# Performance work log

Hardware: AMD Instinct MI355X
Metric: run time of the kernel (lower is better)

## Reference

```python
import jax, jax.numpy as jnp
import numpy as np

BATCH, SEQ, DIN, FILTERS, KSIZE = 64, 512, 256, 256, 3

def setup_inputs() -> dict:
    key = jax.random.key(0)
    ks = jax.random.split(key, 5)
    s_u = 1.0 / np.sqrt(DIN)
    return {
        "x": jax.random.normal(ks[0], (BATCH, SEQ, DIN), dtype=jnp.float32),
        "z": jax.random.normal(ks[1], (BATCH, DIN), dtype=jnp.float32),
        "U": jax.random.normal(ks[2], (DIN, DIN), dtype=jnp.float32) * s_u,
        "V": jax.random.normal(ks[3], (DIN, KSIZE * FILTERS), dtype=jnp.float32) * s_u,
        "B_w": jax.random.normal(ks[4], (DIN, KSIZE * FILTERS), dtype=jnp.float32) * s_u,
        "b": jnp.zeros((FILTERS,), dtype=jnp.float32),
        "kernel_size": KSIZE,
    }

def reference(x, z, U, V, B_w, b, kernel_size):
    Bn, L, din = x.shape
    K = int(kernel_size)
    F = V.shape[1] // K
    # per-sample dynamic kernel: (U * sigmoid(z)) @ V + B
    zf = jax.nn.sigmoid(z)                                  # (B, din)
    f = jnp.einsum('de,be,ef->bdf', U, zf, V) + B_w[None]    # (B, din, K*F)
    f = f.reshape(Bn, din, K, F).transpose(0, 2, 1, 3)       # (B, K, din, F)
    # 'same' padding, stride 1
    pad_l, pad_r = (K - 1) // 2, K // 2
    xp = jnp.pad(x, ((0, 0), (pad_l, pad_r), (0, 0)))        # (B, L+K-1, din)
    patches = jnp.stack([xp[:, i:i + L] for i in range(K)], axis=2)  # (B, L, K, din)
    out = jnp.einsum('blkd,bkdf->blf', patches, f) + b       # (B, L, F)
    return jax.nn.relu(out)
```

## Files before the change

kernel.cpp:

```cpp
#include <hip/hip_runtime.h>
#include <math.h>

#define BATCH 64
#define SEQL  512
#define DIN   256
#define NF    256
#define KS    3
#define KF    (KS * NF)

#define XCH 512
#define XL  (SEQL + 2)
#define KC  (KS * XCH)
#define LDR 128
#define AROWS 136

typedef __attribute__((ext_vector_type(8))) short short8;
typedef __attribute__((ext_vector_type(4))) float floatx4;
typedef __attribute__((ext_vector_type(8))) unsigned short ushort8v;

static __device__ __forceinline__ unsigned short f2bf(float f) {
    unsigned int u = __float_as_uint(f);
    return (unsigned short)((u + 0x7FFF + ((u >> 16) & 1)) >> 16);
}

static __device__ __forceinline__ void gl_lds16(const void* g, void* l) {
    __builtin_amdgcn_global_load_lds(
        (const __attribute__((address_space(1))) unsigned int*)g,
        (__attribute__((address_space(3))) unsigned int*)l, 16, 0, 0);
}

template <int NROWS>
static __device__ __forceinline__ void stage_tile(
    const unsigned short* __restrict__ gbase, size_t rs,
    unsigned short* lds, int wave, int lane)
{
    constexpr int WROWS = NROWS / 4;
    const int rsub = lane >> 4;
    const int ud   = lane & 15;
    unsigned short* ldsw = lds + (size_t)(wave * WROWS) * LDR;
    const unsigned short* g = gbase + (size_t)(wave * WROWS) * rs;
    #pragma unroll
    for (int c = 0; c < WROWS / 4; ++c) {
        const int r  = c * 4 + rsub;
        const int ug = ud ^ (r & 15);
        gl_lds16(g + (size_t)r * rs + ug * 8, ldsw + (size_t)(c * 4) * LDR);
    }
}

__global__ __launch_bounds__(256) void pack_kernel(
    const float* __restrict__ U, const float* __restrict__ V,
    const float* __restrict__ Bw,
    unsigned short* __restrict__ WcT, unsigned short* __restrict__ UT,
    unsigned short* __restrict__ Xc)
{
    const int blk = blockIdx.x;
    const int t   = threadIdx.x;
    __shared__ unsigned short tile[64][64 + 2];

    if (blk < 96) {
        const int f0 = (blk & 3) * 64, c0 = (blk >> 2) * 64;
        const int fl = t & 63, cb = t >> 6;
        #pragma unroll
        for (int it = 0; it < 16; ++it) {
            const int cl = cb + it * 4;
            const int c  = c0 + cl;
            const int k  = c >> 9, ch = c & (XCH - 1);
            const float v = (ch < DIN) ? Bw[(size_t)ch * KF + k * NF + f0 + fl]
                                       : V[(size_t)(ch - DIN) * KF + k * NF + f0 + fl];
            tile[cl][fl] = f2bf(v);
        }
        __syncthreads();
        const int cl2 = t & 63, fb = t >> 6;
        #pragma unroll
        for (int it = 0; it < 16; ++it) {
            const int fl2 = fb + it * 4;
            WcT[(size_t)(f0 + fl2) * KC + c0 + cl2] = tile[cl2][fl2];
        }
    } else if (blk < 112) {
        const int bb = blk - 96;
        const int e0 = (bb & 3) * 64, d0 = (bb >> 2) * 64;
        const int el = t & 63, db = t >> 6;
        #pragma unroll
        for (int it = 0; it < 16; ++it) {
            const int dl = db + it * 4;
            tile[dl][el] = f2bf(U[(size_t)(d0 + dl) * DIN + e0 + el]);
        }
        __syncthreads();
        const int dl2 = t & 63, eb = t >> 6;
        #pragma unroll
        for (int it = 0; it < 16; ++it) {
            const int el2 = eb + it * 4;
            UT[(size_t)(e0 + el2) * DIN + d0 + dl2] = tile[dl2][el2];
        }
    } else {
        const int b = blk - 112;
        unsigned int* r0 = (unsigned int*)(Xc + (size_t)b * XL * XCH);
        unsigned int* r1 = (unsigned int*)(Xc + ((size_t)b * XL + XL - 1) * XCH);
        r0[t] = 0u;
        r1[t] = 0u;
    }
}

__global__ __launch_bounds__(256, 4) void stage1_kernel(
    const float* __restrict__ x, const unsigned short* __restrict__ UT,
    const float* __restrict__ z, unsigned short* __restrict__ Xc)
{
    __shared__ unsigned short sh[16384];
    unsigned short* As = sh;
    unsigned short* Bs = sh + 4096;

    const int tid  = threadIdx.x;
    const int lane = tid & 63;
    const int wave = tid >> 6;
    const int quad = lane >> 4, l16 = lane & 15;

    const int bid   = blockIdx.x;
    const int ft    = (bid >> 3) & 1;
    const int mt    = ((bid >> 4) << 3) | (bid & 7);
    const int b     = mt >> 3;
    const int lbase = (mt & 7) * 64;
    const int e0    = ft * 128;
    const bool writeX = (ft == 0);

    const int r8  = lane >> 3;
    const int ud8 = lane & 7;

    floatx4 acc[4][2] = {};

    for (int k0 = 0; k0 < DIN; k0 += 64) {
        #pragma unroll
        for (int c = 0; c < 4; ++c) {
            const int r  = wave * 32 + c * 8 + r8;
            const int ug = ud8 ^ (r & 7);
            gl_lds16(UT + (size_t)(e0 + r) * DIN + k0 + ug * 8,
                     Bs + (size_t)(wave * 32 + c * 8) * 64);
        }
        #pragma unroll
        for (int it = 0; it < 2; ++it) {
            const int idx = tid + it * 256;
            const int row = idx >> 3;
            const int u   = idx & 7;
            const int ug  = u ^ (row & 7);
            const float* xp =
                x + ((size_t)b * SEQL + lbase + row) * DIN + k0 + ug * 8;
            const float4 v0 = *(const float4*)xp;
            const float4 v1 = *(const float4*)(xp + 4);
            ushort8v h;
            h[0] = f2bf(v0.x); h[1] = f2bf(v0.y); h[2] = f2bf(v0.z); h[3] = f2bf(v0.w);
            h[4] = f2bf(v1.x); h[5] = f2bf(v1.y); h[6] = f2bf(v1.z); h[7] = f2bf(v1.w);
            *(ushort8v*)&As[row * 64 + u * 8] = h;
            if (writeX)
                *(ushort8v*)&Xc[((size_t)b * XL + lbase + 1 + row) * XCH + k0 + ug * 8] = h;
        }
        __syncthreads();

        #pragma unroll
        for (int ks = 0; ks < 2; ++ks) {
            short8 af[4], bfr[2];
            #pragma unroll
            for (int i = 0; i < 4; ++i) {
                const int m = i * 16 + l16;
                af[i] = *(const short8*)&As[m * 64 + (((ks * 4 + quad) ^ (l16 & 7)) * 8)];
            }
            #pragma unroll
            for (int j = 0; j < 2; ++j) {
                const int n = wave * 32 + j * 16 + l16;
                bfr[j] = *(const short8*)&Bs[n * 64 + (((ks * 4 + quad) ^ (l16 & 7)) * 8)];
            }
            #pragma unroll
            for (int i = 0; i < 4; ++i)
                #pragma unroll
                for (int j = 0; j < 2; ++j)
                    acc[i][j] = __builtin_amdgcn_mfma_f32_16x16x32_bf16(
                        af[i], bfr[j], acc[i][j], 0, 0, 0);
        }
        __syncthreads();
    }

    #pragma unroll
    for (int j = 0; j < 2; ++j) {
        const int el = wave * 32 + j * 16 + l16;
        const float zf = 1.0f / (1.0f + expf(-z[(size_t)b * DIN + e0 + el]));
        #pragma unroll
        for (int i = 0; i < 4; ++i) {
            const int m = i * 16 + quad * 4;
            #pragma unroll
            for (int r = 0; r < 4; ++r)
                sh[(m + r) * 128 + el] = f2bf(acc[i][j][r] * zf);
        }
    }
    __syncthreads();
    #pragma unroll
    for (int it = 0; it < 4; ++it) {
        const int idx = tid + it * 256;
        const int row = idx >> 4;
        const int u   = idx & 15;
        *(ushort8v*)&Xc[((size_t)b * XL + lbase + 1 + row) * XCH + DIN + e0 + u * 8] =
            *(const ushort8v*)&sh[row * 128 + u * 8];
    }
}

__global__ __launch_bounds__(256, 3) void stage2_kernel(
    const unsigned short* __restrict__ Xc,
    const unsigned short* __restrict__ WcT,
    const float* __restrict__ bias, float* __restrict__ out)
{
    __shared__ unsigned short As[AROWS * LDR];
    __shared__ unsigned short Bs[64 * LDR];

    const int tid  = threadIdx.x;
    const int lane = tid & 63;
    const int wave = tid >> 6;
    const int quad = lane >> 4, l16 = lane & 15;

    const int bid   = blockIdx.x;
    const int ft    = (bid >> 3) & 3;
    const int mt    = ((bid >> 5) << 3) | (bid & 7);
    const int b     = mt >> 2;
    const int lbase = (mt & 3) * 128;
    const int f0    = ft * 64;

    const unsigned short* gA = Xc + ((size_t)b * XL + lbase) * XCH;
    const unsigned short* gB = WcT + (size_t)f0 * KC;

    const int rsub = lane >> 4;
    const int ud   = lane & 15;
    const int wr0   = (wave < 2) ? wave * 36 : 72 + (wave - 2) * 32;
    const int ncall = (wave < 2) ? 9 : 8;

    floatx4 acc[2][4] = {};

    #pragma unroll 1
    for (int g = 0; g < 4; ++g) {
        #pragma unroll
        for (int c = 0; c < 9; ++c) {
            if (c < ncall) {
                const int r  = wr0 + c * 4 + rsub;
                const int ug = ud ^ (r & 15);
                gl_lds16(gA + (size_t)r * XCH + g * 128 + ug * 8,
                         As + (size_t)(wr0 + c * 4) * LDR);
            }
        }
        #pragma unroll 1
        for (int k = 0; k < KS; ++k) {
            stage_tile<64>(gB + k * XCH + g * 128, KC, Bs, wave, lane);
            __syncthreads();

            #pragma unroll
            for (int ks = 0; ks < 4; ++ks) {
                short8 af[2], bfr[4];
                #pragma unroll
                for (int i = 0; i < 2; ++i) {
                    const int m = wave * 32 + i * 16 + l16;
                    af[i] = *(const short8*)
                        &As[(m + k) * LDR + (((ks * 4 + quad) ^ ((l16 + k) & 15)) * 8)];
                }
                #pragma unroll
                for (int j = 0; j < 4; ++j) {
                    const int n = j * 16 + l16;
                    bfr[j] = *(const short8*)
                        &Bs[n * LDR + (((ks * 4 + quad) ^ l16) * 8)];
                }
                #pragma unroll
                for (int i = 0; i < 2; ++i)
                    #pragma unroll
                    for (int j = 0; j < 4; ++j)
                        acc[i][j] = __builtin_amdgcn_mfma_f32_16x16x32_bf16(
                            af[i], bfr[j], acc[i][j], 0, 0, 0);
            }
            __syncthreads();
        }
    }

    #pragma unroll
    for (int j = 0; j < 4; ++j) {
        const int f  = f0 + j * 16 + l16;
        const float bv = bias[f];
        #pragma unroll
        for (int i = 0; i < 2; ++i) {
            const int lrow = lbase + wave * 32 + i * 16 + quad * 4;
            #pragma unroll
            for (int r = 0; r < 4; ++r) {
                const float v = acc[i][j][r] + bv;
                out[((size_t)b * SEQL + lrow + r) * NF + f] = fmaxf(v, 0.0f);
            }
        }
    }
}

extern "C" void kernel_launch(void* const* d_in, const int* in_sizes, int n_in,
                              void* d_out, int out_size, void* d_ws, size_t ws_size,
                              hipStream_t stream) {
    const float* x    = (const float*)d_in[0];
    const float* z    = (const float*)d_in[1];
    const float* U    = (const float*)d_in[2];
    const float* V    = (const float*)d_in[3];
    const float* Bw   = (const float*)d_in[4];
    const float* bias = (const float*)d_in[5];

    unsigned short* Xc  = (unsigned short*)d_ws;
    unsigned short* WcT = Xc + (size_t)BATCH * XL * XCH;
    unsigned short* UT  = WcT + (size_t)NF * KC;
    float* out = (float*)d_out;

    pack_kernel<<<dim3(176), 256, 0, stream>>>(U, V, Bw, WcT, UT, Xc);
    stage1_kernel<<<dim3(1024), 256, 0, stream>>>(x, UT, z, Xc);
    stage2_kernel<<<dim3(1024), 256, 0, stream>>>(Xc, WcT, bias, out);
}
```

Measured before the change: 137.5 us.

## Fuse stage1 and stage2 into one kernel holding the concatenated input in LDS

Stage1 (x@U scaled by sigmoid(z)) and stage2 (the conv as a GEMM over concatenated [x, xU] channels) are merged into one kernel. Each 512-thread block keeps a 130-row halo tile of bf16 x and the computed projection in LDS, so the Xc intermediate no longer round-trips through global memory and one launch plus the pad-zeroing work go away. In exchange the grid drops from 1024 blocks to 256 large-LDS blocks, which lowers occupancy and parallelism. The halo rows of the projection are also recomputed per block.

```diff
diff --git a/kernel.cpp b/kernel.cpp
--- a/kernel.cpp
+++ b/kernel.cpp
@@ -9,10 +9,10 @@
 #define KF    (KS * NF)
 
 #define XCH 512
-#define XL  (SEQL + 2)
 #define KC  (KS * XCH)
-#define LDR 128
-#define AROWS 136
+#define PROWS 130
+#define PLD   128
+#define PSZ   (PROWS * PLD)
 
 typedef __attribute__((ext_vector_type(8))) short short8;
 typedef __attribute__((ext_vector_type(4))) float floatx4;
@@ -29,29 +29,10 @@
         (__attribute__((address_space(3))) unsigned int*)l, 16, 0, 0);
 }
 
-template <int NROWS>
-static __device__ __forceinline__ void stage_tile(
-    const unsigned short* __restrict__ gbase, size_t rs,
-    unsigned short* lds, int wave, int lane)
-{
-    constexpr int WROWS = NROWS / 4;
-    const int rsub = lane >> 4;
-    const int ud   = lane & 15;
-    unsigned short* ldsw = lds + (size_t)(wave * WROWS) * LDR;
-    const unsigned short* g = gbase + (size_t)(wave * WROWS) * rs;
-    #pragma unroll
-    for (int c = 0; c < WROWS / 4; ++c) {
-        const int r  = c * 4 + rsub;
-        const int ug = ud ^ (r & 15);
-        gl_lds16(g + (size_t)r * rs + ug * 8, ldsw + (size_t)(c * 4) * LDR);
-    }
-}
-
 __global__ __launch_bounds__(256) void pack_kernel(
     const float* __restrict__ U, const float* __restrict__ V,
     const float* __restrict__ Bw,
-    unsigned short* __restrict__ WcT, unsigned short* __restrict__ UT,
-    unsigned short* __restrict__ Xc)
+    unsigned short* __restrict__ WcT, unsigned short* __restrict__ UT)
 {
     const int blk = blockIdx.x;
     const int t   = threadIdx.x;
@@ -76,7 +57,7 @@
             const int fl2 = fb + it * 4;
             WcT[(size_t)(f0 + fl2) * KC + c0 + cl2] = tile[cl2][fl2];
         }
-    } else if (blk < 112) {
+    } else {
         const int bb = blk - 96;
         const int e0 = (bb & 3) * 64, d0 = (bb >> 2) * 64;
         const int el = t & 63, db = t >> 6;
@@ -92,197 +73,161 @@
             const int el2 = eb + it * 4;
             UT[(size_t)(e0 + el2) * DIN + d0 + dl2] = tile[dl2][el2];
         }
-    } else {
-        const int b = blk - 112;
-        unsigned int* r0 = (unsigned int*)(Xc + (size_t)b * XL * XCH);
-        unsigned int* r1 = (unsigned int*)(Xc + ((size_t)b * XL + XL - 1) * XCH);
-        r0[t] = 0u;
-        r1[t] = 0u;
-    }
-}
-
-__global__ __launch_bounds__(256, 4) void stage1_kernel(
-    const float* __restrict__ x, const unsigned short* __restrict__ UT,
-    const float* __restrict__ z, unsigned short* __restrict__ Xc)
+    }
+}
+
+__global__ __launch_bounds__(512, 2) void fused_kernel(
+    const float* __restrict__ x, const float* __restrict__ z,
+    const unsigned short* __restrict__ UT,
+    const unsigned short* __restrict__ WcT,
+    const float* __restrict__ bias, float* __restrict__ out)
 {
-    __shared__ unsigned short sh[16384];
-    unsigned short* As = sh;
-    unsigned short* Bs = sh + 4096;
+    __shared__ unsigned short lds[4 * PSZ + 128 * 64];
+    unsigned short* Bs = lds + 4 * PSZ;
 
     const int tid  = threadIdx.x;
     const int lane = tid & 63;
     const int wave = tid >> 6;
     const int quad = lane >> 4, l16 = lane & 15;
+    const int r8   = lane >> 3, ud8 = lane & 7;
 
     const int bid   = blockIdx.x;
-    const int ft    = (bid >> 3) & 1;
-    const int mt    = ((bid >> 4) << 3) | (bid & 7);
-    const int b     = mt >> 3;
-    const int lbase = (mt & 7) * 64;
-    const int e0    = ft * 128;
-    const bool writeX = (ft == 0);
-
-    const int r8  = lane >> 3;
-    const int ud8 = lane & 7;
-
-    floatx4 acc[4][2] = {};
-
-    for (int k0 = 0; k0 < DIN; k0 += 64) {
-        #pragma unroll
-        for (int c = 0; c < 4; ++c) {
-            const int r  = wave * 32 + c * 8 + r8;
-            const int ug = ud8 ^ (r & 7);
-            gl_lds16(UT + (size_t)(e0 + r) * DIN + k0 + ug * 8,
-                     Bs + (size_t)(wave * 32 + c * 8) * 64);
-        }
-        #pragma unroll
-        for (int it = 0; it < 2; ++it) {
-            const int idx = tid + it * 256;
-            const int row = idx >> 3;
-            const int u   = idx & 7;
-            const int ug  = u ^ (row & 7);
-            const float* xp =
-                x + ((size_t)b * SEQL + lbase + row) * DIN + k0 + ug * 8;
-            const float4 v0 = *(const float4*)xp;
-            const float4 v1 = *(const float4*)(xp + 4);
-            ushort8v h;
-            h[0] = f2bf(v0.x); h[1] = f2bf(v0.y); h[2] = f2bf(v0.z); h[3] = f2bf(v0.w);
-            h[4] = f2bf(v1.x); h[5] = f2bf(v1.y); h[6] = f2bf(v1.z); h[7] = f2bf(v1.w);
-            *(ushort8v*)&As[row * 64 + u * 8] = h;
-            if (writeX)
-                *(ushort8v*)&Xc[((size_t)b * XL + lbase + 1 + row) * XCH + k0 + ug * 8] = h;
-        }
-        __syncthreads();
-
-        #pragma unroll
-        for (int ks = 0; ks < 2; ++ks) {
-            short8 af[4], bfr[2];
-            #pragma unroll
-            for (int i = 0; i < 4; ++i) {
-                const int m = i * 16 + l16;
-                af[i] = *(const short8*)&As[m * 64 + (((ks * 4 + quad) ^ (l16 & 7)) * 8)];
-            }
-            #pragma unroll
-            for (int j = 0; j < 2; ++j) {
-                const int n = wave * 32 + j * 16 + l16;
-                bfr[j] = *(const short8*)&Bs[n * 64 + (((ks * 4 + quad) ^ (l16 & 7)) * 8)];
-            }
-            #pragma unroll
-            for (int i = 0; i < 4; ++i)
+    const int b     = bid >> 2;
+    const int lbase = (bid & 3) * 128;
+
+    #pragma unroll 1
+    for (int p = 0; p < 2; ++p) {
+        unsigned short* P = lds + p * PSZ;
+        #pragma unroll
+        for (int it = 0; it < 5; ++it) {
+            const int idx = tid + it * 512;
+            if (idx < PROWS * 16) {
+                const int row = idx >> 4, u = idx & 15;
+                const int l = lbase - 1 + row;
+                ushort8v h = {};
+                if (l >= 0 && l < SEQL) {
+                    const float* xp = x + ((size_t)b * SEQL + l) * DIN + p * 128 + u * 8;
+                    const float4 v0 = *(const float4*)xp;
+                    const float4 v1 = *(const float4*)(xp + 4);
+                    h[0] = f2bf(v0.x); h[1] = f2bf(v0.y);
+                    h[2] = f2bf(v0.z); h[3] = f2bf(v0.w);
+                    h[4] = f2bf(v1.x); h[5] = f2bf(v1.y);
+                    h[6] = f2bf(v1.z); h[7] = f2bf(v1.w);
+                }
+                *(ushort8v*)&P[row * PLD + ((u ^ (row & 15)) << 3)] = h;
+            }
+        }
+    }
+    __syncthreads();
+
+    #pragma unroll 1
+    for (int eh = 0; eh < 2; ++eh) {
+        floatx4 accY[9] = {};
+        #pragma unroll 1
+        for (int kk = 0; kk < 4; ++kk) {
+            const unsigned short* gU = UT + (size_t)(eh * 128) * DIN + kk * 64;
+            #pragma unroll
+            for (int c = 0; c < 2; ++c) {
+                const int r = wave * 16 + c * 8 + r8;
+                gl_lds16(gU + (size_t)r * DIN + (ud8 ^ (r & 7)) * 8,
+                         Bs + (size_t)(wave * 16 + c * 8) * 64);
+            }
+            __syncthreads();
+            const unsigned short* P = lds + (kk >> 1) * PSZ;
+            const int dh = kk & 1;
+            #pragma unroll
+            for (int ks = 0; ks < 2; ++ks) {
+                const short8 bf = *(const short8*)
+                    &Bs[(wave * 16 + l16) * 64 + (((ks * 4 + quad) ^ (l16 & 7)) * 8)];
                 #pragma unroll
-                for (int j = 0; j < 2; ++j)
-                    acc[i][j] = __builtin_amdgcn_mfma_f32_16x16x32_bf16(
-                        af[i], bfr[j], acc[i][j], 0, 0, 0);
-        }
-        __syncthreads();
-    }
-
-    #pragma unroll
-    for (int j = 0; j < 2; ++j) {
-        const int el = wave * 32 + j * 16 + l16;
-        const float zf = 1.0f / (1.0f + expf(-z[(size_t)b * DIN + e0 + el]));
-        #pragma unroll
-        for (int i = 0; i < 4; ++i) {
-            const int m = i * 16 + quad * 4;
-            #pragma unroll
-            for (int r = 0; r < 4; ++r)
-                sh[(m + r) * 128 + el] = f2bf(acc[i][j][r] * zf);
+                for (int i = 0; i < 9; ++i) {
+                    const short8 af = *(const short8*)
+                        &P[(i * 16 + l16) * PLD +
+                           (((dh * 8 + ks * 4 + quad) ^ (l16 & 15)) * 8)];
+                    accY[i] = __builtin_amdgcn_mfma_f32_16x16x32_bf16(
+                        af, bf, accY[i], 0, 0, 0);
+                }
+            }
+            __syncthreads();
+        }
+        const int ecol = wave * 16 + l16;
+        const float zf = 1.0f /
+            (1.0f + expf(-z[(size_t)b * DIN + eh * 128 + ecol]));
+        unsigned short* PY = lds + (2 + eh) * PSZ;
+        const int u16e = ecol >> 3;
+        #pragma unroll
+        for (int i = 0; i < 9; ++i) {
+            #pragma unroll
+            for (int r = 0; r < 4; ++r) {
+                const int row = i * 16 + quad * 4 + r;
+                if (row < PROWS)
+                    PY[row * PLD + ((u16e ^ (row & 15)) << 3) + (ecol & 7)] =
+                        f2bf(accY[i][r] * zf);
+            }
         }
     }
     __syncthreads();
-    #pragma unroll
-    for (int it = 0; it < 4; ++it) {
-        const int idx = tid + it * 256;
-        const int row = idx >> 4;
-        const int u   = idx & 15;
-        *(ushort8v*)&Xc[((size_t)b * XL + lbase + 1 + row) * XCH + DIN + e0 + u * 8] =
-            *(const ushort8v*)&sh[row * 128 + u * 8];
-    }
-}
-
-__global__ __launch_bounds__(256, 3) void stage2_kernel(
-    const unsigned short* __restrict__ Xc,
-    const unsigned short* __restrict__ WcT,
-    const float* __restrict__ bias, float* __restrict__ out)
-{
-    __shared__ unsigned short As[AROWS * LDR];
-    __shared__ unsigned short Bs[64 * LDR];
-
-    const int tid  = threadIdx.x;
-    const int lane = tid & 63;
-    const int wave = tid >> 6;
-    const int quad = lane >> 4, l16 = lane & 15;
-
-    const int bid   = blockIdx.x;
-    const int ft    = (bid >> 3) & 3;
-    const int mt    = ((bid >> 5) << 3) | (bid & 7);
-    const int b     = mt >> 2;
-    const int lbase = (mt & 3) * 128;
-    const int f0    = ft * 64;
-
-    const unsigned short* gA = Xc + ((size_t)b * XL + lbase) * XCH;
-    const unsigned short* gB = WcT + (size_t)f0 * KC;
-
-    const int rsub = lane >> 4;
-    const int ud   = lane & 15;
-    const int wr0   = (wave < 2) ? wave * 36 : 72 + (wave - 2) * 32;
-    const int ncall = (wave < 2) ? 9 : 8;
-
-    floatx4 acc[2][4] = {};
-
+
+    const int wr = wave & 3;
+    const int wc = wave >> 2;
     #pragma unroll 1
-    for (int g = 0; g < 4; ++g) {
-        #pragma unroll
-        for (int c = 0; c < 9; ++c) {
-            if (c < ncall) {
-                const int r  = wr0 + c * 4 + rsub;
-                const int ug = ud ^ (r & 15);
-                gl_lds16(gA + (size_t)r * XCH + g * 128 + ug * 8,
-                         As + (size_t)(wr0 + c * 4) * LDR);
-            }
-        }
+    for (int fh = 0; fh < 2; ++fh) {
+        floatx4 acc[2][4] = {};
         #pragma unroll 1
-        for (int k = 0; k < KS; ++k) {
-            stage_tile<64>(gB + k * XCH + g * 128, KC, Bs, wave, lane);
-            __syncthreads();
-
-            #pragma unroll
-            for (int ks = 0; ks < 4; ++ks) {
-                short8 af[2], bfr[4];
+        for (int g = 0; g < 4; ++g) {
+            const unsigned short* P = lds + g * PSZ;
+            #pragma unroll 1
+            for (int k = 0; k < KS; ++k) {
+                #pragma unroll 1
+                for (int hh = 0; hh < 2; ++hh) {
+                    const unsigned short* gW =
+                        WcT + (size_t)(fh * 128) * KC + k * XCH + g * 128 + hh * 64;
+                    #pragma unroll
+                    for (int c = 0; c < 2; ++c) {
+                        const int r = wave * 16 + c * 8 + r8;
+                        gl_lds16(gW + (size_t)r * KC + (ud8 ^ (r & 7)) * 8,
+                                 Bs + (size_t)(wave * 16 + c * 8) * 64);
+                    }
+                    __syncthreads();
+                    #pragma unroll
+                    for (int ks = 0; ks < 2; ++ks) {
+                        short8 af[2], bfr[4];
+                        #pragma unroll
+                        for (int i = 0; i < 2; ++i) {
+                            const int row = wr * 32 + i * 16 + l16 + k;
+                            af[i] = *(const short8*)
+                                &P[row * PLD +
+                                   (((hh * 8 + ks * 4 + quad) ^ (row & 15)) * 8)];
+                        }
+                        #pragma unroll
+                        for (int j = 0; j < 4; ++j) {
+                            const int n = wc * 64 + j * 16 + l16;
+                            bfr[j] = *(const short8*)
+                                &Bs[n * 64 + (((ks * 4 + quad) ^ (n & 7)) * 8)];
+                        }
+                        #pragma unroll
+                        for (int i = 0; i < 2; ++i)
+                            #pragma unroll
+                            for (int j = 0; j < 4; ++j)
+                                acc[i][j] = __builtin_amdgcn_mfma_f32_16x16x32_bf16(
+                                    af[i], bfr[j], acc[i][j], 0, 0, 0);
+                    }
+                    __syncthreads();
+                }
+            }
+        }
+        #pragma unroll
+        for (int j = 0; j < 4; ++j) {
+            const int f  = fh * 128 + wc * 64 + j * 16 + l16;
+            const float bv = bias[f];
+            #pragma unroll
+            for (int i = 0; i < 2; ++i) {
+                const int lrow = lbase + wr * 32 + i * 16 + quad * 4;
                 #pragma unroll
-                for (int i = 0; i < 2; ++i) {
-                    const int m = wave * 32 + i * 16 + l16;
-                    af[i] = *(const short8*)
-                        &As[(m + k) * LDR + (((ks * 4 + quad) ^ ((l16 + k) & 15)) * 8)];
-                }
-                #pragma unroll
-                for (int j = 0; j < 4; ++j) {
-                    const int n = j * 16 + l16;
-                    bfr[j] = *(const short8*)
-                        &Bs[n * LDR + (((ks * 4 + quad) ^ l16) * 8)];
-                }
-                #pragma unroll
-                for (int i = 0; i < 2; ++i)
-                    #pragma unroll
-                    for (int j = 0; j < 4; ++j)
-                        acc[i][j] = __builtin_amdgcn_mfma_f32_16x16x32_bf16(
-                            af[i], bfr[j], acc[i][j], 0, 0, 0);
-            }
-            __syncthreads();
-        }
-    }
-
-    #pragma unroll
-    for (int j = 0; j < 4; ++j) {
-        const int f  = f0 + j * 16 + l16;
-        const float bv = bias[f];
-        #pragma unroll
-        for (int i = 0; i < 2; ++i) {
-            const int lrow = lbase + wave * 32 + i * 16 + quad * 4;
-            #pragma unroll
-            for (int r = 0; r < 4; ++r) {
-                const float v = acc[i][j][r] + bv;
-                out[((size_t)b * SEQL + lrow + r) * NF + f] = fmaxf(v, 0.0f);
+                for (int r = 0; r < 4; ++r) {
+                    const float v = acc[i][j][r] + bv;
+                    out[((size_t)b * SEQL + lrow + r) * NF + f] = fmaxf(v, 0.0f);
+                }
             }
         }
     }
@@ -298,12 +243,10 @@
     const float* Bw   = (const float*)d_in[4];
     const float* bias = (const float*)d_in[5];
 
-    unsigned short* Xc  = (unsigned short*)d_ws;
-    unsigned short* WcT = Xc + (size_t)BATCH * XL * XCH;
+    unsigned short* WcT = (unsigned short*)d_ws;
     unsigned short* UT  = WcT + (size_t)NF * KC;
     float* out = (float*)d_out;
 
-    pack_kernel<<<dim3(176), 256, 0, stream>>>(U, V, Bw, WcT, UT, Xc);
-    stage1_kernel<<<dim3(1024), 256, 0, stream>>>(x, UT, z, Xc);
-    stage2_kernel<<<dim3(1024), 256, 0, stream>>>(Xc, WcT, bias, out);
-}
+    pack_kernel<<<dim3(112), 256, 0, stream>>>(U, V, Bw, WcT, UT);
+    fused_kernel<<<dim3(256), 512, 0, stream>>>(x, z, UT, WcT, bias, out);
+}
```

New measurement: 148.7 us. +8.2%, slower.
